# Optimization experiments

Measured on AMD Instinct MI355X. Metric: run time of the kernel, lower is better.

The kernel has to match this reference:

```python
import jax, jax.numpy as jnp
import numpy as np

N = 100000
E = 1600000
D_IN = 128
D_HID = 128
D_OUT = 128


def _glorot(key, shape):
    fan_in, fan_out = shape[1], shape[0]
    lim = np.sqrt(6.0 / (fan_in + fan_out)).astype(np.float32)
    return jax.random.uniform(key, shape, jnp.float32, -lim, lim)


def setup_inputs() -> dict:
    key = jax.random.key(0)
    ks = jax.random.split(key, 8)
    x = jax.random.normal(ks[0], (N, D_IN), jnp.float32)
    edge_index = jax.random.randint(ks[1], (2, E), 0, N, jnp.int64)
    # SAGEConv params: lin_l acts on aggregated neighbors (has bias), lin_r on root.
    W1l = _glorot(ks[2], (D_HID, D_IN))
    W1r = _glorot(ks[3], (D_HID, D_IN))
    b1 = jnp.zeros((D_HID,), jnp.float32)
    W2l = _glorot(ks[4], (D_OUT, D_HID))
    W2r = _glorot(ks[5], (D_OUT, D_HID))
    b2 = jnp.zeros((D_OUT,), jnp.float32)
    return {"x": x, "edge_index": edge_index,
            "W1l": W1l, "W1r": W1r, "b1": b1,
            "W2l": W2l, "W2r": W2r, "b2": b2}


def _sage_conv(x, src, dst, Wl, Wr, b):
    # mean-aggregate neighbor features j->i, then lin_l(mean) + lin_r(x) + b
    msgs = x[src]                                             # [E, d]
    summed = jax.ops.segment_sum(msgs, dst, num_segments=N)   # [N, d]
    deg = jax.ops.segment_sum(jnp.ones((src.shape[0],), x.dtype), dst,
                              num_segments=N)                 # [N]
    mean = summed / jnp.maximum(deg, 1.0)[:, None]
    return mean @ Wl.T + x @ Wr.T + b


def reference(x, edge_index, W1l, W1r, b1, W2l, W2r, b2):
    src, dst = edge_index[0], edge_index[1]
    h = jax.nn.relu(_sage_conv(x, src, dst, W1l, W1r, b1))
    # dropout p=0.2 is identity in eval mode
    out = _sage_conv(h, src, dst, W2l, W2r, b2)
    return out
```

## Files before the change

kernel.cpp:

```cpp
#include <hip/hip_runtime.h>

#define N_NODES 100000
#define N_EDGES 1600000
#define D 128
#define NBUCK 782
#define BSTRIDE 2560
#define EPB 4096

typedef __attribute__((ext_vector_type(8))) short short8v;
typedef __attribute__((ext_vector_type(4))) float f32x4;

__device__ __forceinline__ unsigned short f2bf(float f) {
    unsigned int u = __float_as_uint(f);
    unsigned int r = (u + 0x7fffu + ((u >> 16) & 1u)) >> 16;
    return (unsigned short)r;
}
__device__ __forceinline__ float bf2f(unsigned int lo16) {
    return __uint_as_float(lo16 << 16);
}
__device__ __forceinline__ short8v zero8() {
    short8v z = {0, 0, 0, 0, 0, 0, 0, 0};
    return z;
}

__global__ void k_prep(const float* __restrict__ W1l, const float* __restrict__ W1r,
                       const float* __restrict__ W2l, const float* __restrict__ W2r,
                       unsigned short* __restrict__ wc1, unsigned short* __restrict__ wc2,
                       int* __restrict__ gcnt) {
    int idx = blockIdx.x * 256 + threadIdx.x;
    if (idx < 16384)       wc1[idx] = f2bf(W1l[idx]);
    else if (idx < 32768)  wc1[idx] = f2bf(W1r[idx - 16384]);
    else if (idx < 65536) {
        int j = idx - 32768;
        int o = j >> 8, k2 = j & 255;
        float v = (k2 < 128) ? W2l[o * 128 + k2] : W2r[o * 128 + (k2 - 128)];
        wc2[j] = f2bf(v);
    }
    else if (idx - 65536 < NBUCK) gcnt[idx - 65536] = 0;
}

__global__ __launch_bounds__(256) void k_bscatter(const int* __restrict__ src,
                                                  const int* __restrict__ dst,
                                                  int* __restrict__ gcnt,
                                                  unsigned int* __restrict__ ebuf) {
    __shared__ int cnt[NBUCK];
    __shared__ int base[NBUCK];
    const int t = threadIdx.x;
    const int e0 = blockIdx.x * EPB;
    for (int i = t; i < NBUCK; i += 256) cnt[i] = 0;
    __syncthreads();
#pragma unroll
    for (int u = 0; u < EPB / 256; ++u) {
        int e = e0 + u * 256 + t;
        if (e < N_EDGES) atomicAdd(&cnt[dst[e] >> 7], 1);
    }
    __syncthreads();
    for (int i = t; i < NBUCK; i += 256) {
        int c = cnt[i];
        base[i] = c ? atomicAdd(&gcnt[i], c) : 0;
        cnt[i] = 0;
    }
    __syncthreads();
#pragma unroll
    for (int u = 0; u < EPB / 256; ++u) {
        int e = e0 + u * 256 + t;
        if (e < N_EDGES) {
            int d = dst[e];
            int b = d >> 7;
            int pos = b * BSTRIDE + base[b] + atomicAdd(&cnt[b], 1);
            ebuf[pos] = ((unsigned int)(d & 127) << 17) | (unsigned int)src[e];
        }
    }
}

__global__ __launch_bounds__(256) void k_bsort(const unsigned int* __restrict__ ebuf,
                                               const int* __restrict__ gcnt,
                                               int* __restrict__ row_start,
                                               int* __restrict__ ssrc) {
    __shared__ int h[128];
    __shared__ int sc[128];
    const int b = blockIdx.x;
    const int t = threadIdx.x;
    const int eb = b * BSTRIDE;
    const int n = gcnt[b];
    if (t < 128) h[t] = 0;
    __syncthreads();
    for (int e = t; e < n; e += 256)
        atomicAdd(&h[ebuf[eb + e] >> 17], 1);
    __syncthreads();
    if (t < 128) sc[t] = h[t];
    __syncthreads();
    for (int o = 1; o < 128; o <<= 1) {
        int add = 0;
        if (t < 128 && t >= o) add = sc[t - o];
        __syncthreads();
        if (t < 128) sc[t] += add;
        __syncthreads();
    }
    if (t < 128) {
        int excl = sc[t] - h[t];
        row_start[b * 129 + t] = eb + excl;
        h[t] = excl;
    }
    if (t == 0) row_start[b * 129 + 128] = eb + n;
    __syncthreads();
    for (int e = t; e < n; e += 256) {
        unsigned int pk = ebuf[eb + e];
        int dl = pk >> 17;
        int pos = eb + atomicAdd(&h[dl], 1);
        ssrc[pos] = (int)(pk & 0x1ffffu);
    }
}

__global__ __launch_bounds__(256) void k_gemm1(
    const float* __restrict__ Af,
    const unsigned short* __restrict__ Bt,
    const float* __restrict__ bias,
    unsigned short* __restrict__ Tout,
    unsigned short* __restrict__ Hout)
{
    const int wid = threadIdx.x >> 6;
    const int lane = threadIdx.x & 63;
    const int l15 = lane & 15, lg = lane >> 4;
    const int col_base = wid * 64;

    short8v bfrag[4][4];
#pragma unroll
    for (int cg = 0; cg < 4; ++cg)
#pragma unroll
        for (int ks = 0; ks < 4; ++ks)
            bfrag[cg][ks] = *(const short8v*)&Bt[(size_t)(col_base + cg * 16 + l15) * 128
                                                 + ks * 32 + lg * 8];
    float bv[4];
#pragma unroll
    for (int cg = 0; cg < 4; ++cg)
        bv[cg] = (wid >= 2) ? bias[(wid - 2) * 64 + cg * 16 + l15] : 0.0f;

    const int ntiles = (N_NODES + 63) / 64;
    for (int tile = blockIdx.x; tile < ntiles; tile += gridDim.x) {
        const int row0 = tile * 64;
        f32x4 acc[4][4];
#pragma unroll
        for (int rg = 0; rg < 4; ++rg)
#pragma unroll
            for (int cg = 0; cg < 4; ++cg)
                acc[rg][cg] = (f32x4){0.f, 0.f, 0.f, 0.f};

#pragma unroll
        for (int rg = 0; rg < 4; ++rg) {
            const int arow = row0 + rg * 16 + l15;
            short8v afrag[4];
            if (arow < N_NODES) {
#pragma unroll
                for (int ks = 0; ks < 4; ++ks) {
                    float4 p0 = *(const float4*)&Af[(size_t)arow * 128 + ks * 32 + lg * 8];
                    float4 p1 = *(const float4*)&Af[(size_t)arow * 128 + ks * 32 + lg * 8 + 4];
                    short8v f;
                    f[0] = (short)f2bf(p0.x); f[1] = (short)f2bf(p0.y);
                    f[2] = (short)f2bf(p0.z); f[3] = (short)f2bf(p0.w);
                    f[4] = (short)f2bf(p1.x); f[5] = (short)f2bf(p1.y);
                    f[6] = (short)f2bf(p1.z); f[7] = (short)f2bf(p1.w);
                    afrag[ks] = f;
                }
            } else {
#pragma unroll
                for (int ks = 0; ks < 4; ++ks) afrag[ks] = zero8();
            }
#pragma unroll
            for (int cg = 0; cg < 4; ++cg)
#pragma unroll
                for (int ks = 0; ks < 4; ++ks)
                    acc[rg][cg] = __builtin_amdgcn_mfma_f32_16x16x32_bf16(
                        afrag[ks], bfrag[cg][ks], acc[rg][cg], 0, 0, 0);
        }

        unsigned short* outp = (wid < 2) ? Tout : Hout;
        const int cb = (wid < 2) ? col_base : col_base - 128;
        const bool addb = (wid >= 2);
#pragma unroll
        for (int rg = 0; rg < 4; ++rg) {
            const int rbase = row0 + rg * 16 + lg * 4;
#pragma unroll
            for (int cg = 0; cg < 4; ++cg) {
                const int col = cb + cg * 16 + l15;
#pragma unroll
                for (int i = 0; i < 4; ++i) {
                    int row = rbase + i;
                    if (row < N_NODES) {
                        float v = acc[rg][cg][i] + (addb ? bv[cg] : 0.0f);
                        outp[(size_t)row * 128 + col] = f2bf(v);
                    }
                }
            }
        }
    }
}

__global__ __launch_bounds__(256) void k_gemm2(
    const unsigned short* __restrict__ M,
    const unsigned short* __restrict__ H,
    const unsigned short* __restrict__ Bt,
    const float* __restrict__ bias,
    float* __restrict__ out)
{
    const int wid = threadIdx.x >> 6;
    const int lane = threadIdx.x & 63;
    const int l15 = lane & 15, lg = lane >> 4;
    const int col_base = wid * 32;

    short8v bfrag[2][8];
#pragma unroll
    for (int cg = 0; cg < 2; ++cg)
#pragma unroll
        for (int ks = 0; ks < 8; ++ks)
            bfrag[cg][ks] = *(const short8v*)&Bt[(size_t)(col_base + cg * 16 + l15) * 256
                                                 + ks * 32 + lg * 8];
    float bv[2];
#pragma unroll
    for (int cg = 0; cg < 2; ++cg)
        bv[cg] = bias[col_base + cg * 16 + l15];

    const int ntiles = (N_NODES + 63) / 64;
    for (int tile = blockIdx.x; tile < ntiles; tile += gridDim.x) {
        const int row0 = tile * 64;
        f32x4 acc[4][2];
#pragma unroll
        for (int rg = 0; rg < 4; ++rg)
#pragma unroll
            for (int cg = 0; cg < 2; ++cg)
                acc[rg][cg] = (f32x4){0.f, 0.f, 0.f, 0.f};

#pragma unroll
        for (int rg = 0; rg < 4; ++rg) {
            const int arow = row0 + rg * 16 + l15;
            short8v afrag[8];
            if (arow < N_NODES) {
#pragma unroll
                for (int ks = 0; ks < 4; ++ks) {
                    afrag[ks]     = *(const short8v*)&M[(size_t)arow * 128 + ks * 32 + lg * 8];
                    afrag[ks + 4] = *(const short8v*)&H[(size_t)arow * 128 + ks * 32 + lg * 8];
                }
            } else {
#pragma unroll
                for (int ks = 0; ks < 8; ++ks) afrag[ks] = zero8();
            }
#pragma unroll
            for (int cg = 0; cg < 2; ++cg)
#pragma unroll
                for (int ks = 0; ks < 8; ++ks)
                    acc[rg][cg] = __builtin_amdgcn_mfma_f32_16x16x32_bf16(
                        afrag[ks], bfrag[cg][ks], acc[rg][cg], 0, 0, 0);
        }

#pragma unroll
        for (int rg = 0; rg < 4; ++rg) {
            const int rbase = row0 + rg * 16 + lg * 4;
#pragma unroll
            for (int cg = 0; cg < 2; ++cg) {
                const int col = col_base + cg * 16 + l15;
#pragma unroll
                for (int i = 0; i < 4; ++i) {
                    int row = rbase + i;
                    if (row < N_NODES)
                        out[(size_t)row * 128 + col] = acc[rg][cg][i] + bv[cg];
                }
            }
        }
    }
}

template <bool RMW>
__global__ __launch_bounds__(256) void k_agg(
    const unsigned short* __restrict__ t_mat,
    const int* __restrict__ ssrc,
    const int* __restrict__ row_start,
    unsigned short* __restrict__ io)
{
    int w = (blockIdx.x * blockDim.x + threadIdx.x) >> 6;
    int lane = threadIdx.x & 63;
    if (w >= N_NODES) return;
    const int b = w >> 7, dl = w & 127;
    const int rs = row_start[b * 129 + dl];
    const int re = row_start[b * 129 + dl + 1];
    const int d = re - rs;
    const int half = lane >> 5;
    const int l31 = lane & 31;

    uint2 cur;
    cur.x = 0u; cur.y = 0u;
    if (RMW && lane < 32)
        cur = *((const uint2*)io + (size_t)w * 32 + l31);

    const uint2* tlane = (const uint2*)t_mat + l31;
    float a0 = 0.f, a1 = 0.f, a2 = 0.f, a3 = 0.f;

    for (int q0 = rs; q0 < re; q0 += 64) {
        int nb = 0;
        if (q0 + lane < re) nb = ssrc[q0 + lane];
        const int m = min(64, re - q0);
        int q = 0;
        for (; q + 16 <= m; q += 16) {
            uint2 v[8];
#pragma unroll
            for (int u = 0; u < 8; ++u) {
                int j = __shfl(nb, q + u * 2 + half);
                v[u] = tlane[(size_t)j * 32];
            }
#pragma unroll
            for (int u = 0; u < 8; ++u) {
                a0 += bf2f(v[u].x & 0xffffu);
                a1 += __uint_as_float(v[u].x & 0xffff0000u);
                a2 += bf2f(v[u].y & 0xffffu);
                a3 += __uint_as_float(v[u].y & 0xffff0000u);
            }
        }
        for (; q + 2 <= m; q += 2) {
            int j = __shfl(nb, q + half);
            uint2 vv = tlane[(size_t)j * 32];
            a0 += bf2f(vv.x & 0xffffu);
            a1 += __uint_as_float(vv.x & 0xffff0000u);
            a2 += bf2f(vv.y & 0xffffu);
            a3 += __uint_as_float(vv.y & 0xffff0000u);
        }
        if (q < m) {
            int j = __shfl(nb, q);
            if (half == 0) {
                uint2 vv = tlane[(size_t)j * 32];
                a0 += bf2f(vv.x & 0xffffu);
                a1 += __uint_as_float(vv.x & 0xffff0000u);
                a2 += bf2f(vv.y & 0xffffu);
                a3 += __uint_as_float(vv.y & 0xffff0000u);
            }
        }
    }

    a0 += __shfl_xor(a0, 32);
    a1 += __shfl_xor(a1, 32);
    a2 += __shfl_xor(a2, 32);
    a3 += __shfl_xor(a3, 32);

    if (lane < 32) {
        const float inv = 1.0f / (float)max(d, 1);
        float r0, r1, r2, r3;
        if (RMW) {
            r0 = fmaxf(bf2f(cur.x & 0xffffu) + inv * a0, 0.f);
            r1 = fmaxf(__uint_as_float(cur.x & 0xffff0000u) + inv * a1, 0.f);
            r2 = fmaxf(bf2f(cur.y & 0xffffu) + inv * a2, 0.f);
            r3 = fmaxf(__uint_as_float(cur.y & 0xffff0000u) + inv * a3, 0.f);
        } else {
            r0 = inv * a0; r1 = inv * a1; r2 = inv * a2; r3 = inv * a3;
        }
        uint2 o;
        o.x = (unsigned int)f2bf(r0) | ((unsigned int)f2bf(r1) << 16);
        o.y = (unsigned int)f2bf(r2) | ((unsigned int)f2bf(r3) << 16);
        *((uint2*)io + (size_t)w * 32 + l31) = o;
    }
}


extern "C" void kernel_launch(void* const* d_in, const int* in_sizes, int n_in,
                              void* d_out, int out_size, void* d_ws, size_t ws_size,
                              hipStream_t stream) {
    const float* x   = (const float*)d_in[0];
    const int*   ei  = (const int*)d_in[1];
    const float* W1l = (const float*)d_in[2];
    const float* W1r = (const float*)d_in[3];
    const float* b1  = (const float*)d_in[4];
    const float* W2l = (const float*)d_in[5];
    const float* W2r = (const float*)d_in[6];
    const float* b2  = (const float*)d_in[7];
    float* out = (float*)d_out;

    const int* src = ei;
    const int* dst = ei + N_EDGES;

    char* p = (char*)d_ws;
    auto alloc = [&](size_t bytes) {
        char* r = p;
        p += (bytes + 255) & ~(size_t)255;
        return r;
    };
    unsigned short* tb = (unsigned short*)alloc((size_t)N_NODES * D * 2);
    unsigned short* hx = (unsigned short*)alloc((size_t)N_NODES * D * 2);
    unsigned int*   ebuf = (unsigned int*)alloc((size_t)NBUCK * BSTRIDE * 4);
    int*   ssrc      = (int*)alloc((size_t)NBUCK * BSTRIDE * 4);
    int*   gcnt      = (int*)alloc(NBUCK * sizeof(int));
    int*   row_start = (int*)alloc((size_t)NBUCK * 129 * sizeof(int));
    unsigned short* wc1 = (unsigned short*)alloc(256 * 128 * 2);
    unsigned short* wc2 = (unsigned short*)alloc(128 * 256 * 2);

    k_prep<<<(65536 + NBUCK + 255) / 256, 256, 0, stream>>>(W1l, W1r, W2l, W2r, wc1, wc2, gcnt);
    k_bscatter<<<(N_EDGES + EPB - 1) / EPB, 256, 0, stream>>>(src, dst, gcnt, ebuf);
    k_bsort<<<NBUCK, 256, 0, stream>>>(ebuf, gcnt, row_start, ssrc);

    const int agg_grid = (N_NODES + 3) / 4;

    k_gemm1<<<640, 256, 0, stream>>>(x, wc1, b1, tb, hx);
    k_agg<true><<<agg_grid, 256, 0, stream>>>(tb, ssrc, row_start, hx);

    k_agg<false><<<agg_grid, 256, 0, stream>>>(hx, ssrc, row_start, tb);
    k_gemm2<<<640, 256, 0, stream>>>(tb, hx, wc2, b2, out);
}
```

Measured before the change: 250.0 us.

## Fuse gemm1 with edge bucket scatter and drop weight prep kernel

Merges the first GEMM and the edge bucket-scatter into one launch whose blocks split by blockIdx, so the two independent jobs run concurrently. The weight-prep kernel is removed: each block converts fp32 weights to bf16 in registers, and the bucket counters are zeroed with hipMemsetAsync. Both GEMMs switch from persistent 640-block loops to one tile per block, and conversions use the packed bf16 intrinsics. This cuts launch count and per-element conversion cost, at the price of redundant weight loads and conversion in every block.

```diff
diff --git a/kernel.cpp b/kernel.cpp
--- a/kernel.cpp
+++ b/kernel.cpp
@@ -1,4 +1,5 @@
 #include <hip/hip_runtime.h>
+#include <hip/hip_bf16.h>
 
 #define N_NODES 100000
 #define N_EDGES 1600000
@@ -6,6 +7,8 @@
 #define NBUCK 782
 #define BSTRIDE 2560
 #define EPB 4096
+#define G1_TILES 1563
+#define SC_BLOCKS ((N_EDGES + EPB - 1) / EPB)
 
 typedef __attribute__((ext_vector_type(8))) short short8v;
 typedef __attribute__((ext_vector_type(4))) float f32x4;
@@ -22,53 +25,125 @@
     short8v z = {0, 0, 0, 0, 0, 0, 0, 0};
     return z;
 }
-
-__global__ void k_prep(const float* __restrict__ W1l, const float* __restrict__ W1r,
-                       const float* __restrict__ W2l, const float* __restrict__ W2r,
-                       unsigned short* __restrict__ wc1, unsigned short* __restrict__ wc2,
-                       int* __restrict__ gcnt) {
-    int idx = blockIdx.x * 256 + threadIdx.x;
-    if (idx < 16384)       wc1[idx] = f2bf(W1l[idx]);
-    else if (idx < 32768)  wc1[idx] = f2bf(W1r[idx - 16384]);
-    else if (idx < 65536) {
-        int j = idx - 32768;
-        int o = j >> 8, k2 = j & 255;
-        float v = (k2 < 128) ? W2l[o * 128 + k2] : W2r[o * 128 + (k2 - 128)];
-        wc2[j] = f2bf(v);
-    }
-    else if (idx - 65536 < NBUCK) gcnt[idx - 65536] = 0;
-}
-
-__global__ __launch_bounds__(256) void k_bscatter(const int* __restrict__ src,
-                                                  const int* __restrict__ dst,
-                                                  int* __restrict__ gcnt,
-                                                  unsigned int* __restrict__ ebuf) {
-    __shared__ int cnt[NBUCK];
-    __shared__ int base[NBUCK];
-    const int t = threadIdx.x;
-    const int e0 = blockIdx.x * EPB;
-    for (int i = t; i < NBUCK; i += 256) cnt[i] = 0;
-    __syncthreads();
-#pragma unroll
-    for (int u = 0; u < EPB / 256; ++u) {
-        int e = e0 + u * 256 + t;
-        if (e < N_EDGES) atomicAdd(&cnt[dst[e] >> 7], 1);
-    }
-    __syncthreads();
-    for (int i = t; i < NBUCK; i += 256) {
-        int c = cnt[i];
-        base[i] = c ? atomicAdd(&gcnt[i], c) : 0;
-        cnt[i] = 0;
-    }
-    __syncthreads();
-#pragma unroll
-    for (int u = 0; u < EPB / 256; ++u) {
-        int e = e0 + u * 256 + t;
-        if (e < N_EDGES) {
-            int d = dst[e];
-            int b = d >> 7;
-            int pos = b * BSTRIDE + base[b] + atomicAdd(&cnt[b], 1);
-            ebuf[pos] = ((unsigned int)(d & 127) << 17) | (unsigned int)src[e];
+__device__ __forceinline__ short8v cvt8(const float4 p0, const float4 p1) {
+    union { __hip_bfloat162 h[4]; short8v s; } u;
+    u.h[0] = __float22bfloat162_rn(make_float2(p0.x, p0.y));
+    u.h[1] = __float22bfloat162_rn(make_float2(p0.z, p0.w));
+    u.h[2] = __float22bfloat162_rn(make_float2(p1.x, p1.y));
+    u.h[3] = __float22bfloat162_rn(make_float2(p1.z, p1.w));
+    return u.s;
+}
+
+__global__ __launch_bounds__(256) void k_fused1(
+    const float* __restrict__ Af,
+    const float* __restrict__ W1l, const float* __restrict__ W1r,
+    const float* __restrict__ bias,
+    unsigned short* __restrict__ Tout,
+    unsigned short* __restrict__ Hout,
+    const int* __restrict__ src, const int* __restrict__ dst,
+    int* __restrict__ gcnt, unsigned int* __restrict__ ebuf)
+{
+    if (blockIdx.x >= G1_TILES) {
+        __shared__ int cnt[NBUCK];
+        __shared__ int base[NBUCK];
+        const int t = threadIdx.x;
+        const int e0 = (blockIdx.x - G1_TILES) * EPB;
+        for (int i = t; i < NBUCK; i += 256) cnt[i] = 0;
+        __syncthreads();
+#pragma unroll
+        for (int u = 0; u < EPB / 256; ++u) {
+            int e = e0 + u * 256 + t;
+            if (e < N_EDGES) atomicAdd(&cnt[dst[e] >> 7], 1);
+        }
+        __syncthreads();
+        for (int i = t; i < NBUCK; i += 256) {
+            int c = cnt[i];
+            base[i] = c ? atomicAdd(&gcnt[i], c) : 0;
+            cnt[i] = 0;
+        }
+        __syncthreads();
+#pragma unroll
+        for (int u = 0; u < EPB / 256; ++u) {
+            int e = e0 + u * 256 + t;
+            if (e < N_EDGES) {
+                int d = dst[e];
+                int b = d >> 7;
+                int pos = b * BSTRIDE + base[b] + atomicAdd(&cnt[b], 1);
+                ebuf[pos] = ((unsigned int)(d & 127) << 17) | (unsigned int)src[e];
+            }
+        }
+        return;
+    }
+
+    const int wid = threadIdx.x >> 6;
+    const int lane = threadIdx.x & 63;
+    const int l15 = lane & 15, lg = lane >> 4;
+    const int col_base = wid * 64;
+
+    short8v bfrag[4][4];
+#pragma unroll
+    for (int cg = 0; cg < 4; ++cg) {
+        const int row = col_base + cg * 16 + l15;
+        const float* wrow = (row < 128) ? &W1l[(size_t)row * 128]
+                                        : &W1r[(size_t)(row - 128) * 128];
+#pragma unroll
+        for (int ks = 0; ks < 4; ++ks) {
+            const int k0 = ks * 32 + lg * 8;
+            bfrag[cg][ks] = cvt8(*(const float4*)&wrow[k0],
+                                 *(const float4*)&wrow[k0 + 4]);
+        }
+    }
+    float bv[4];
+#pragma unroll
+    for (int cg = 0; cg < 4; ++cg)
+        bv[cg] = (wid >= 2) ? bias[(wid - 2) * 64 + cg * 16 + l15] : 0.0f;
+
+    const int row0 = blockIdx.x * 64;
+    f32x4 acc[4][4];
+#pragma unroll
+    for (int rg = 0; rg < 4; ++rg)
+#pragma unroll
+        for (int cg = 0; cg < 4; ++cg)
+            acc[rg][cg] = (f32x4){0.f, 0.f, 0.f, 0.f};
+
+#pragma unroll
+    for (int rg = 0; rg < 4; ++rg) {
+        const int arow = row0 + rg * 16 + l15;
+        short8v afrag[4];
+        if (arow < N_NODES) {
+#pragma unroll
+            for (int ks = 0; ks < 4; ++ks)
+                afrag[ks] = cvt8(*(const float4*)&Af[(size_t)arow * 128 + ks * 32 + lg * 8],
+                                 *(const float4*)&Af[(size_t)arow * 128 + ks * 32 + lg * 8 + 4]);
+        } else {
+#pragma unroll
+            for (int ks = 0; ks < 4; ++ks) afrag[ks] = zero8();
+        }
+#pragma unroll
+        for (int cg = 0; cg < 4; ++cg)
+#pragma unroll
+            for (int ks = 0; ks < 4; ++ks)
+                acc[rg][cg] = __builtin_amdgcn_mfma_f32_16x16x32_bf16(
+                    afrag[ks], bfrag[cg][ks], acc[rg][cg], 0, 0, 0);
+    }
+
+    unsigned short* outp = (wid < 2) ? Tout : Hout;
+    const int cb = (wid < 2) ? col_base : col_base - 128;
+    const bool addb = (wid >= 2);
+#pragma unroll
+    for (int rg = 0; rg < 4; ++rg) {
+        const int rbase = row0 + rg * 16 + lg * 4;
+#pragma unroll
+        for (int cg = 0; cg < 4; ++cg) {
+            const int col = cb + cg * 16 + l15;
+#pragma unroll
+            for (int i = 0; i < 4; ++i) {
+                int row = rbase + i;
+                if (row < N_NODES) {
+                    float v = acc[rg][cg][i] + (addb ? bv[cg] : 0.0f);
+                    *(__hip_bfloat16*)&outp[(size_t)row * 128 + col] = __float2bfloat16(v);
+                }
+            }
         }
     }
 }
@@ -112,94 +187,10 @@
     }
 }
 
-__global__ __launch_bounds__(256) void k_gemm1(
-    const float* __restrict__ Af,
-    const unsigned short* __restrict__ Bt,
-    const float* __restrict__ bias,
-    unsigned short* __restrict__ Tout,
-    unsigned short* __restrict__ Hout)
-{
-    const int wid = threadIdx.x >> 6;
-    const int lane = threadIdx.x & 63;
-    const int l15 = lane & 15, lg = lane >> 4;
-    const int col_base = wid * 64;
-
-    short8v bfrag[4][4];
-#pragma unroll
-    for (int cg = 0; cg < 4; ++cg)
-#pragma unroll
-        for (int ks = 0; ks < 4; ++ks)
-            bfrag[cg][ks] = *(const short8v*)&Bt[(size_t)(col_base + cg * 16 + l15) * 128
-                                                 + ks * 32 + lg * 8];
-    float bv[4];
-#pragma unroll
-    for (int cg = 0; cg < 4; ++cg)
-        bv[cg] = (wid >= 2) ? bias[(wid - 2) * 64 + cg * 16 + l15] : 0.0f;
-
-    const int ntiles = (N_NODES + 63) / 64;
-    for (int tile = blockIdx.x; tile < ntiles; tile += gridDim.x) {
-        const int row0 = tile * 64;
-        f32x4 acc[4][4];
-#pragma unroll
-        for (int rg = 0; rg < 4; ++rg)
-#pragma unroll
-            for (int cg = 0; cg < 4; ++cg)
-                acc[rg][cg] = (f32x4){0.f, 0.f, 0.f, 0.f};
-
-#pragma unroll
-        for (int rg = 0; rg < 4; ++rg) {
-            const int arow = row0 + rg * 16 + l15;
-            short8v afrag[4];
-            if (arow < N_NODES) {
-#pragma unroll
-                for (int ks = 0; ks < 4; ++ks) {
-                    float4 p0 = *(const float4*)&Af[(size_t)arow * 128 + ks * 32 + lg * 8];
-                    float4 p1 = *(const float4*)&Af[(size_t)arow * 128 + ks * 32 + lg * 8 + 4];
-                    short8v f;
-                    f[0] = (short)f2bf(p0.x); f[1] = (short)f2bf(p0.y);
-                    f[2] = (short)f2bf(p0.z); f[3] = (short)f2bf(p0.w);
-                    f[4] = (short)f2bf(p1.x); f[5] = (short)f2bf(p1.y);
-                    f[6] = (short)f2bf(p1.z); f[7] = (short)f2bf(p1.w);
-                    afrag[ks] = f;
-                }
-            } else {
-#pragma unroll
-                for (int ks = 0; ks < 4; ++ks) afrag[ks] = zero8();
-            }
-#pragma unroll
-            for (int cg = 0; cg < 4; ++cg)
-#pragma unroll
-                for (int ks = 0; ks < 4; ++ks)
-                    acc[rg][cg] = __builtin_amdgcn_mfma_f32_16x16x32_bf16(
-                        afrag[ks], bfrag[cg][ks], acc[rg][cg], 0, 0, 0);
-        }
-
-        unsigned short* outp = (wid < 2) ? Tout : Hout;
-        const int cb = (wid < 2) ? col_base : col_base - 128;
-        const bool addb = (wid >= 2);
-#pragma unroll
-        for (int rg = 0; rg < 4; ++rg) {
-            const int rbase = row0 + rg * 16 + lg * 4;
-#pragma unroll
-            for (int cg = 0; cg < 4; ++cg) {
-                const int col = cb + cg * 16 + l15;
-#pragma unroll
-                for (int i = 0; i < 4; ++i) {
-                    int row = rbase + i;
-                    if (row < N_NODES) {
-                        float v = acc[rg][cg][i] + (addb ? bv[cg] : 0.0f);
-                        outp[(size_t)row * 128 + col] = f2bf(v);
-                    }
-                }
-            }
-        }
-    }
-}
-
 __global__ __launch_bounds__(256) void k_gemm2(
     const unsigned short* __restrict__ M,
     const unsigned short* __restrict__ H,
-    const unsigned short* __restrict__ Bt,
+    const float* __restrict__ W2l, const float* __restrict__ W2r,
     const float* __restrict__ bias,
     float* __restrict__ out)
 {
@@ -210,60 +201,63 @@
 
     short8v bfrag[2][8];
 #pragma unroll
-    for (int cg = 0; cg < 2; ++cg)
-#pragma unroll
-        for (int ks = 0; ks < 8; ++ks)
-            bfrag[cg][ks] = *(const short8v*)&Bt[(size_t)(col_base + cg * 16 + l15) * 256
-                                                 + ks * 32 + lg * 8];
+    for (int cg = 0; cg < 2; ++cg) {
+        const int o = col_base + cg * 16 + l15;
+        const float* wl = &W2l[(size_t)o * 128];
+        const float* wr = &W2r[(size_t)o * 128];
+#pragma unroll
+        for (int ks = 0; ks < 4; ++ks) {
+            const int k0 = ks * 32 + lg * 8;
+            bfrag[cg][ks]     = cvt8(*(const float4*)&wl[k0], *(const float4*)&wl[k0 + 4]);
+            bfrag[cg][ks + 4] = cvt8(*(const float4*)&wr[k0], *(const float4*)&wr[k0 + 4]);
+        }
+    }
     float bv[2];
 #pragma unroll
     for (int cg = 0; cg < 2; ++cg)
         bv[cg] = bias[col_base + cg * 16 + l15];
 
-    const int ntiles = (N_NODES + 63) / 64;
-    for (int tile = blockIdx.x; tile < ntiles; tile += gridDim.x) {
-        const int row0 = tile * 64;
-        f32x4 acc[4][2];
-#pragma unroll
-        for (int rg = 0; rg < 4; ++rg)
-#pragma unroll
-            for (int cg = 0; cg < 2; ++cg)
-                acc[rg][cg] = (f32x4){0.f, 0.f, 0.f, 0.f};
-
-#pragma unroll
-        for (int rg = 0; rg < 4; ++rg) {
-            const int arow = row0 + rg * 16 + l15;
-            short8v afrag[8];
-            if (arow < N_NODES) {
-#pragma unroll
-                for (int ks = 0; ks < 4; ++ks) {
-                    afrag[ks]     = *(const short8v*)&M[(size_t)arow * 128 + ks * 32 + lg * 8];
-                    afrag[ks + 4] = *(const short8v*)&H[(size_t)arow * 128 + ks * 32 + lg * 8];
-                }
-            } else {
-#pragma unroll
-                for (int ks = 0; ks < 8; ++ks) afrag[ks] = zero8();
-            }
-#pragma unroll
-            for (int cg = 0; cg < 2; ++cg)
-#pragma unroll
-                for (int ks = 0; ks < 8; ++ks)
-                    acc[rg][cg] = __builtin_amdgcn_mfma_f32_16x16x32_bf16(
-                        afrag[ks], bfrag[cg][ks], acc[rg][cg], 0, 0, 0);
-        }
-
-#pragma unroll
-        for (int rg = 0; rg < 4; ++rg) {
-            const int rbase = row0 + rg * 16 + lg * 4;
-#pragma unroll
-            for (int cg = 0; cg < 2; ++cg) {
-                const int col = col_base + cg * 16 + l15;
-#pragma unroll
-                for (int i = 0; i < 4; ++i) {
-                    int row = rbase + i;
-                    if (row < N_NODES)
-                        out[(size_t)row * 128 + col] = acc[rg][cg][i] + bv[cg];
-                }
+    const int row0 = blockIdx.x * 64;
+    f32x4 acc[4][2];
+#pragma unroll
+    for (int rg = 0; rg < 4; ++rg)
+#pragma unroll
+        for (int cg = 0; cg < 2; ++cg)
+            acc[rg][cg] = (f32x4){0.f, 0.f, 0.f, 0.f};
+
+#pragma unroll
+    for (int rg = 0; rg < 4; ++rg) {
+        const int arow = row0 + rg * 16 + l15;
+        short8v afrag[8];
+        if (arow < N_NODES) {
+#pragma unroll
+            for (int ks = 0; ks < 4; ++ks) {
+                afrag[ks]     = *(const short8v*)&M[(size_t)arow * 128 + ks * 32 + lg * 8];
+                afrag[ks + 4] = *(const short8v*)&H[(size_t)arow * 128 + ks * 32 + lg * 8];
+            }
+        } else {
+#pragma unroll
+            for (int ks = 0; ks < 8; ++ks) afrag[ks] = zero8();
+        }
+#pragma unroll
+        for (int cg = 0; cg < 2; ++cg)
+#pragma unroll
+            for (int ks = 0; ks < 8; ++ks)
+                acc[rg][cg] = __builtin_amdgcn_mfma_f32_16x16x32_bf16(
+                    afrag[ks], bfrag[cg][ks], acc[rg][cg], 0, 0, 0);
+    }
+
+#pragma unroll
+    for (int rg = 0; rg < 4; ++rg) {
+        const int rbase = row0 + rg * 16 + lg * 4;
+#pragma unroll
+        for (int cg = 0; cg < 2; ++cg) {
+            const int col = col_base + cg * 16 + l15;
+#pragma unroll
+            for (int i = 0; i < 4; ++i) {
+                int row = rbase + i;
+                if (row < N_NODES)
+                    out[(size_t)row * 128 + col] = acc[rg][cg][i] + bv[cg];
             }
         }
     }
@@ -386,18 +380,16 @@
     int*   ssrc      = (int*)alloc((size_t)NBUCK * BSTRIDE * 4);
     int*   gcnt      = (int*)alloc(NBUCK * sizeof(int));
     int*   row_start = (int*)alloc((size_t)NBUCK * 129 * sizeof(int));
-    unsigned short* wc1 = (unsigned short*)alloc(256 * 128 * 2);
-    unsigned short* wc2 = (unsigned short*)alloc(128 * 256 * 2);
-
-    k_prep<<<(65536 + NBUCK + 255) / 256, 256, 0, stream>>>(W1l, W1r, W2l, W2r, wc1, wc2, gcnt);
-    k_bscatter<<<(N_EDGES + EPB - 1) / EPB, 256, 0, stream>>>(src, dst, gcnt, ebuf);
+
+    hipMemsetAsync(gcnt, 0, NBUCK * sizeof(int), stream);
+    k_fused1<<<G1_TILES + SC_BLOCKS, 256, 0, stream>>>(x, W1l, W1r, b1, tb, hx,
+                                                       src, dst, gcnt, ebuf);
     k_bsort<<<NBUCK, 256, 0, stream>>>(ebuf, gcnt, row_start, ssrc);
 
     const int agg_grid = (N_NODES + 3) / 4;
 
-    k_gemm1<<<640, 256, 0, stream>>>(x, wc1, b1, tb, hx);
     k_agg<true><<<agg_grid, 256, 0, stream>>>(tb, ssrc, row_start, hx);
 
     k_agg<false><<<agg_grid, 256, 0, stream>>>(hx, ssrc, row_start, tb);
-    k_gemm2<<<640, 256, 0, stream>>>(tb, hx, wc2, b2, out);
-}
+    k_gemm2<<<G1_TILES, 256, 0, stream>>>(tb, hx, W2l, W2r, b2, out);
+}
```

Result: slower. 271.1 us (+8.4%).
